# Kernel optimization log

Measured on AMD Instinct MI355X. Metric: run time of the kernel, lower is better.

The kernel has to match this reference:

```python
import jax, jax.numpy as jnp
import numpy as np

B, S, D, H, K = 64, 512, 256, 4, 1  # batch, seq, dim, heads, seeds; key_dim == D (Keras quirk)
EPS = 1e-6


def setup_inputs() -> dict:
    key = jax.random.key(0)
    ks = jax.random.split(key, 12)
    s = 1.0 / np.sqrt(D)
    return {
        "x": jax.random.normal(ks[0], (B, S, D), jnp.float32),
        "mask": jax.random.randint(ks[1], (B, S), 0, 2, jnp.int32),
        "seeds": jax.random.normal(ks[2], (K, D), jnp.float32) * s,
        "Wq": jax.random.normal(ks[3], (D, H, D), jnp.float32) * s,
        "bq": jnp.zeros((H, D), jnp.float32),
        "Wk": jax.random.normal(ks[4], (D, H, D), jnp.float32) * s,
        "bk": jnp.zeros((H, D), jnp.float32),
        "Wv": jax.random.normal(ks[5], (D, H, D), jnp.float32) * s,
        "bv": jnp.zeros((H, D), jnp.float32),
        "Wo": jax.random.normal(ks[6], (H, D, D), jnp.float32) * s,
        "bo": jnp.zeros((D,), jnp.float32),
        "gamma": jnp.ones((D,), jnp.float32),
        "beta": jnp.zeros((D,), jnp.float32),
    }


def reference(x, mask, seeds, Wq, bq, Wk, bk, Wv, bv, Wo, bo, gamma, beta):
    # Projections (Keras MHA: per-head dim = key_dim = D)
    q = jnp.einsum("kd,dhe->khe", seeds, Wq) + bq           # [K,H,D] (shared across batch)
    kp = jnp.einsum("bsd,dhe->bshe", x, Wk) + bk            # [B,S,H,D]
    vp = jnp.einsum("bsd,dhe->bshe", x, Wv) + bv            # [B,S,H,D]
    scores = jnp.einsum("khe,bshe->bhks", q, kp) / jnp.sqrt(jnp.float32(D))  # [B,H,K,S]
    adder = (1.0 - mask.astype(scores.dtype))[:, None, None, :] * -1e9
    attn = jax.nn.softmax(scores + adder, axis=-1)
    o = jnp.einsum("bhks,bshe->bkhe", attn, vp)             # [B,K,H,D]
    h = jnp.einsum("bkhe,hed->bkd", o, Wo) + bo             # attention output
    h = seeds[None] + h                                     # residual (dropout off: inference)
    mu = jnp.mean(h, axis=-1, keepdims=True)
    var = jnp.mean(jnp.square(h - mu), axis=-1, keepdims=True)
    h = (h - mu) / jnp.sqrt(var + EPS) * gamma + beta
    return h[:, 0, :]                                       # [B,D]
```

## Files before the change

### kernel.cpp

```cpp
#include <hip/hip_runtime.h>
#include <hip/hip_bf16.h>
#include <math.h>

#define BB 64
#define SS 512
#define DD 256
#define HH 4
#define SCALE 0.0625f
#define PAD 261

__device__ inline float wave_red_sum(float v) {
#pragma unroll
    for (int off = 32; off > 0; off >>= 1) v += __shfl_xor(v, off, 64);
    return v;
}
__device__ inline float wave_red_max(float v) {
#pragma unroll
    for (int off = 32; off > 0; off >>= 1) v = fmaxf(v, __shfl_xor(v, off, 64));
    return v;
}

__global__ __launch_bounds__(256) void qp_kernel(const float* __restrict__ seeds,
                                                 const float* __restrict__ Wq,
                                                 float* __restrict__ qp) {
    int c = blockIdx.x, tid = threadIdx.x;
    __shared__ float sl[16];
    if (tid < 16) sl[tid] = seeds[c * 16 + tid];
    __syncthreads();
#pragma unroll
    for (int rep = 0; rep < 4; ++rep) {
        int i = tid + rep * 256;
        float acc = 0.f;
#pragma unroll
        for (int dl = 0; dl < 16; ++dl)
            acc += sl[dl] * Wq[(size_t)(c * 16 + dl) * (HH * DD) + i];
        qp[c * (HH * DD) + i] = acc;
    }
}

__global__ __launch_bounds__(256) void kqf_kernel(const float* __restrict__ Wk,
                                                  const float* __restrict__ bk,
                                                  const float* __restrict__ bq,
                                                  const float* __restrict__ qp,
                                                  float* __restrict__ kqf,
                                                  float* __restrict__ kbg) {
    int h = blockIdx.x >> 2, ds = blockIdx.x & 3;
    int tid = threadIdx.x, w = tid >> 6, lane = tid & 63;
    __shared__ float ql[DD];
    __shared__ float red[4][64];
    __shared__ float rb[4];
    float qv = bq[h * DD + tid];
#pragma unroll
    for (int c = 0; c < 16; ++c) qv += qp[c * (HH * DD) + h * DD + tid];
    ql[tid] = qv;
    float bkv = bk[h * DD + tid] * qv;
    float t1 = wave_red_sum(bkv);
    if (lane == 0) rb[w] = t1;
    __syncthreads();
    if (tid == 0) kbg[h] = rb[0] + rb[1] + rb[2] + rb[3];
    int dl = tid & 63, ec = tid >> 6;
    int d = ds * 64 + dl;
    const float4* wrow = reinterpret_cast<const float4*>(Wk + (size_t)d * (HH * DD) + h * DD + ec * 64);
    const float4* qq4 = reinterpret_cast<const float4*>(&ql[ec * 64]);
    float acc = 0.f;
#pragma unroll
    for (int e4 = 0; e4 < 16; ++e4) {
        float4 wv = wrow[e4], qq = qq4[e4];
        acc += wv.x * qq.x + wv.y * qq.y + wv.z * qq.z + wv.w * qq.w;
    }
    red[ec][dl] = acc;
    __syncthreads();
    if (tid < 64) kqf[h * DD + ds * 64 + tid] = red[0][tid] + red[1][tid] + red[2][tid] + red[3][tid];
}

__global__ __launch_bounds__(256) void flash_kernel(const float* __restrict__ x,
                                                    const int* __restrict__ mask,
                                                    const float* __restrict__ kqg,
                                                    const float* __restrict__ kbg,
                                                    float* __restrict__ xp,
                                                    float* __restrict__ mt,
                                                    float* __restrict__ lt) {
    int b = blockIdx.x >> 3, st = blockIdx.x & 7;
    int tid = threadIdx.x, w = tid >> 6, lane = tid & 63;
    __shared__ float xt[64][PAD];
    __shared__ __align__(16) float part[4][2][64];
    float* sc = &part[0][0][0];

    const float4* xg = reinterpret_cast<const float4*>(x + ((size_t)b * SS + st * 64) * DD);
#pragma unroll
    for (int c = 0; c < 16; ++c) {
        int f = c * 256 + tid;
        float4 v = xg[f];
        int row = f >> 6, col = (f & 63) * 4;
        xt[row][col + 0] = v.x;
        xt[row][col + 1] = v.y;
        xt[row][col + 2] = v.z;
        xt[row][col + 3] = v.w;
    }
    __syncthreads();

    int s = lane;
    int hp = w >> 1, kk = w & 1;
    int off = __builtin_amdgcn_readfirstlane(hp * 2 * DD + kk * 128);
    const float* kA = kqg + off;
    const float* kB = kqg + off + DD;
    const float* xrow = &xt[s][kk * 128];
    float a0 = 0.f, a1 = 0.f;
#pragma unroll 16
    for (int k = 0; k < 128; ++k) {
        float xv = xrow[k];
        a0 = fmaf(xv, kA[k], a0);
        a1 = fmaf(xv, kB[k], a1);
    }
    part[w][0][s] = a0;
    part[w][1][s] = a1;
    __syncthreads();

    int h = w;
    float v = part[2 * (h >> 1)][h & 1][s] + part[2 * (h >> 1) + 1][h & 1][s];
    float score = (v + kbg[h]) * SCALE + (1.f - (float)mask[b * SS + st * 64 + s]) * -1e9f;
    float m = wave_red_max(score);
    float p = __expf(score - m);
    float l = wave_red_sum(p);
    __syncthreads();
    sc[h * 64 + s] = p;
    if (lane == 0) {
        mt[blockIdx.x * 4 + h] = m;
        lt[blockIdx.x * 4 + h] = l;
    }
    __syncthreads();

    float o0 = 0.f, o1 = 0.f, o2 = 0.f, o3 = 0.f;
#pragma unroll 4
    for (int sb = 0; sb < 16; ++sb) {
        float4 p0 = *reinterpret_cast<const float4*>(&sc[0 * 64 + 4 * sb]);
        float4 p1 = *reinterpret_cast<const float4*>(&sc[1 * 64 + 4 * sb]);
        float4 p2 = *reinterpret_cast<const float4*>(&sc[2 * 64 + 4 * sb]);
        float4 p3 = *reinterpret_cast<const float4*>(&sc[3 * 64 + 4 * sb]);
#pragma unroll
        for (int j = 0; j < 4; ++j) {
            float xv = xt[4 * sb + j][tid];
            float pj0 = (j == 0) ? p0.x : (j == 1) ? p0.y : (j == 2) ? p0.z : p0.w;
            float pj1 = (j == 0) ? p1.x : (j == 1) ? p1.y : (j == 2) ? p1.z : p1.w;
            float pj2 = (j == 0) ? p2.x : (j == 1) ? p2.y : (j == 2) ? p2.z : p2.w;
            float pj3 = (j == 0) ? p3.x : (j == 1) ? p3.y : (j == 2) ? p3.z : p3.w;
            o0 = fmaf(pj0, xv, o0);
            o1 = fmaf(pj1, xv, o1);
            o2 = fmaf(pj2, xv, o2);
            o3 = fmaf(pj3, xv, o3);
        }
    }
    float* xpo = xp + (size_t)blockIdx.x * 4 * DD;
    xpo[0 * DD + tid] = o0;
    xpo[1 * DD + tid] = o1;
    xpo[2 * DD + tid] = o2;
    xpo[3 * DD + tid] = o3;
}

__global__ __launch_bounds__(256) void ovwo_kernel(const float* __restrict__ xp,
                                                   const float* __restrict__ mt,
                                                   const float* __restrict__ lt,
                                                   const float* __restrict__ Wv,
                                                   const float* __restrict__ bv,
                                                   const float* __restrict__ Wo,
                                                   float* __restrict__ wop) {
    int b = blockIdx.x >> 2, h = blockIdx.x & 3;
    int tid = threadIdx.x;
    __shared__ float xl[DD];
    __shared__ float ol[DD];
    float M = -3.0e38f;
#pragma unroll
    for (int t = 0; t < 8; ++t) M = fmaxf(M, mt[(b * 8 + t) * 4 + h]);
    float L = 0.f;
    float co[8];
#pragma unroll
    for (int t = 0; t < 8; ++t) {
        co[t] = __expf(mt[(b * 8 + t) * 4 + h] - M);
        L += lt[(b * 8 + t) * 4 + h] * co[t];
    }
    float invL = 1.0f / L;
    float xb = 0.f;
#pragma unroll
    for (int t = 0; t < 8; ++t) xb += co[t] * xp[((size_t)(b * 8 + t) * 4 + h) * DD + tid];
    xl[tid] = xb * invL;
    __syncthreads();
    float acc = bv[h * DD + tid];
    const float* wv = Wv + h * DD + tid;
#pragma unroll 8
    for (int d = 0; d < DD; ++d) acc += xl[d] * wv[(size_t)d * (HH * DD)];
    ol[tid] = acc;
    __syncthreads();
    float a2 = 0.f;
    const float* wo = Wo + (size_t)(h * DD) * DD + tid;
#pragma unroll 8
    for (int e = 0; e < DD; ++e) a2 += ol[e] * wo[(size_t)e * DD];
    wop[((size_t)(b * HH + h)) * DD + tid] = a2;
}

__global__ __launch_bounds__(256) void ln_kernel(const float* __restrict__ wop,
                                                 const float* __restrict__ bo,
                                                 const float* __restrict__ seeds,
                                                 const float* __restrict__ gamma,
                                                 const float* __restrict__ beta,
                                                 float* __restrict__ out) {
    __shared__ float r1[4], r2[4];
    int b = blockIdx.x, tid = threadIdx.x;
    int w = tid >> 6, lane = tid & 63;
    float acc = bo[tid] + seeds[tid];
#pragma unroll
    for (int h = 0; h < HH; ++h) acc += wop[((size_t)(b * HH + h)) * DD + tid];

    float t = wave_red_sum(acc);
    if (lane == 0) r1[w] = t;
    __syncthreads();
    float mu = (r1[0] + r1[1] + r1[2] + r1[3]) * (1.0f / DD);
    float dv = acc - mu;
    float t2 = wave_red_sum(dv * dv);
    if (lane == 0) r2[w] = t2;
    __syncthreads();
    float var = (r2[0] + r2[1] + r2[2] + r2[3]) * (1.0f / DD);
    out[(size_t)b * DD + tid] = dv * rsqrtf(var + 1e-6f) * gamma[tid] + beta[tid];
}

extern "C" void kernel_launch(void* const* d_in, const int* in_sizes, int n_in,
                              void* d_out, int out_size, void* d_ws, size_t ws_size,
                              hipStream_t stream) {
    const float* x = (const float*)d_in[0];
    const int* mask = (const int*)d_in[1];
    const float* seeds = (const float*)d_in[2];
    const float* Wq = (const float*)d_in[3];
    const float* bq = (const float*)d_in[4];
    const float* Wk = (const float*)d_in[5];
    const float* bk = (const float*)d_in[6];
    const float* Wv = (const float*)d_in[7];
    const float* bv = (const float*)d_in[8];
    const float* Wo = (const float*)d_in[9];
    const float* bo = (const float*)d_in[10];
    const float* gamma = (const float*)d_in[11];
    const float* beta = (const float*)d_in[12];
    float* out = (float*)d_out;

    float* ws = (float*)d_ws;
    float* qp  = ws;
    float* kqf = ws + 16384;
    float* kbg = ws + 17408;
    float* mt  = ws + 17424;
    float* lt  = ws + 19472;
    float* xp  = ws + 21520;
    float* wop = ws + 545808;

    qp_kernel<<<16, 256, 0, stream>>>(seeds, Wq, qp);
    kqf_kernel<<<16, 256, 0, stream>>>(Wk, bk, bq, qp, kqf, kbg);
    flash_kernel<<<BB * 8, 256, 0, stream>>>(x, mask, kqf, kbg, xp, mt, lt);
    ovwo_kernel<<<BB * HH, 256, 0, stream>>>(xp, mt, lt, Wv, bv, Wo, wop);
    ln_kernel<<<BB, 256, 0, stream>>>(wop, bo, seeds, gamma, beta, out);
}
```

Measured before the change: 140.7 us.

## Fuse all five stages into one cooperative kernel with grid syncs

Merges the query projection, key-query fold, flash partial attention, value/output projection and layernorm into one cooperative kernel of 512 blocks, separated by grid-wide barriers. The x tile load now overlaps the query/key folding done by the first 16 blocks. The separate qp stage is merged into the kqf stage, so each of those 16 blocks computes its full query projection over all 256 seed dimensions. This is meant to remove four kernel launch gaps and the tail latency between them. In exchange it adds grid.sync costs, depends on all 512 blocks being co-resident, and leaves most blocks idle during the later stages.

```diff
diff --git a/kernel.cpp b/kernel.cpp
--- a/kernel.cpp
+++ b/kernel.cpp
@@ -1,6 +1,8 @@
 #include <hip/hip_runtime.h>
-#include <hip/hip_bf16.h>
+#include <hip/hip_cooperative_groups.h>
 #include <math.h>
+
+namespace cg = cooperative_groups;
 
 #define BB 64
 #define SS 512
@@ -20,70 +22,27 @@
     return v;
 }
 
-__global__ __launch_bounds__(256) void qp_kernel(const float* __restrict__ seeds,
-                                                 const float* __restrict__ Wq,
-                                                 float* __restrict__ qp) {
-    int c = blockIdx.x, tid = threadIdx.x;
-    __shared__ float sl[16];
-    if (tid < 16) sl[tid] = seeds[c * 16 + tid];
-    __syncthreads();
-#pragma unroll
-    for (int rep = 0; rep < 4; ++rep) {
-        int i = tid + rep * 256;
-        float acc = 0.f;
-#pragma unroll
-        for (int dl = 0; dl < 16; ++dl)
-            acc += sl[dl] * Wq[(size_t)(c * 16 + dl) * (HH * DD) + i];
-        qp[c * (HH * DD) + i] = acc;
-    }
-}
-
-__global__ __launch_bounds__(256) void kqf_kernel(const float* __restrict__ Wk,
-                                                  const float* __restrict__ bk,
-                                                  const float* __restrict__ bq,
-                                                  const float* __restrict__ qp,
-                                                  float* __restrict__ kqf,
-                                                  float* __restrict__ kbg) {
-    int h = blockIdx.x >> 2, ds = blockIdx.x & 3;
-    int tid = threadIdx.x, w = tid >> 6, lane = tid & 63;
-    __shared__ float ql[DD];
+__global__ __launch_bounds__(256) void fused_kernel(
+    const float* __restrict__ x, const int* __restrict__ mask,
+    const float* __restrict__ seeds,
+    const float* __restrict__ Wq, const float* __restrict__ bq,
+    const float* __restrict__ Wk, const float* __restrict__ bk,
+    const float* __restrict__ Wv, const float* __restrict__ bv,
+    const float* __restrict__ Wo, const float* __restrict__ bo,
+    const float* __restrict__ gamma, const float* __restrict__ beta,
+    float* __restrict__ out,
+    float* __restrict__ kqf, float* __restrict__ kbg,
+    float* __restrict__ xp, float* __restrict__ mt, float* __restrict__ lt,
+    float* __restrict__ wop) {
+    cg::grid_group grid = cg::this_grid();
+    int blk = blockIdx.x, tid = threadIdx.x, w = tid >> 6, lane = tid & 63;
+    int b = blk >> 3, st = blk & 7;
+
+    __shared__ __align__(16) float xt[64][PAD];
+    __shared__ __align__(16) float part[4][2][64];
+    __shared__ __align__(16) float ql[DD];
     __shared__ float red[4][64];
     __shared__ float rb[4];
-    float qv = bq[h * DD + tid];
-#pragma unroll
-    for (int c = 0; c < 16; ++c) qv += qp[c * (HH * DD) + h * DD + tid];
-    ql[tid] = qv;
-    float bkv = bk[h * DD + tid] * qv;
-    float t1 = wave_red_sum(bkv);
-    if (lane == 0) rb[w] = t1;
-    __syncthreads();
-    if (tid == 0) kbg[h] = rb[0] + rb[1] + rb[2] + rb[3];
-    int dl = tid & 63, ec = tid >> 6;
-    int d = ds * 64 + dl;
-    const float4* wrow = reinterpret_cast<const float4*>(Wk + (size_t)d * (HH * DD) + h * DD + ec * 64);
-    const float4* qq4 = reinterpret_cast<const float4*>(&ql[ec * 64]);
-    float acc = 0.f;
-#pragma unroll
-    for (int e4 = 0; e4 < 16; ++e4) {
-        float4 wv = wrow[e4], qq = qq4[e4];
-        acc += wv.x * qq.x + wv.y * qq.y + wv.z * qq.z + wv.w * qq.w;
-    }
-    red[ec][dl] = acc;
-    __syncthreads();
-    if (tid < 64) kqf[h * DD + ds * 64 + tid] = red[0][tid] + red[1][tid] + red[2][tid] + red[3][tid];
-}
-
-__global__ __launch_bounds__(256) void flash_kernel(const float* __restrict__ x,
-                                                    const int* __restrict__ mask,
-                                                    const float* __restrict__ kqg,
-                                                    const float* __restrict__ kbg,
-                                                    float* __restrict__ xp,
-                                                    float* __restrict__ mt,
-                                                    float* __restrict__ lt) {
-    int b = blockIdx.x >> 3, st = blockIdx.x & 7;
-    int tid = threadIdx.x, w = tid >> 6, lane = tid & 63;
-    __shared__ float xt[64][PAD];
-    __shared__ __align__(16) float part[4][2][64];
     float* sc = &part[0][0][0];
 
     const float4* xg = reinterpret_cast<const float4*>(x + ((size_t)b * SS + st * 64) * DD);
@@ -97,129 +56,147 @@
         xt[row][col + 2] = v.z;
         xt[row][col + 3] = v.w;
     }
-    __syncthreads();
-
-    int s = lane;
-    int hp = w >> 1, kk = w & 1;
-    int off = __builtin_amdgcn_readfirstlane(hp * 2 * DD + kk * 128);
-    const float* kA = kqg + off;
-    const float* kB = kqg + off + DD;
-    const float* xrow = &xt[s][kk * 128];
-    float a0 = 0.f, a1 = 0.f;
+
+    if (blk < 16) {
+        int h = blk >> 2, ds = blk & 3;
+        float qv = bq[h * DD + tid];
+#pragma unroll 8
+        for (int d = 0; d < DD; ++d)
+            qv = fmaf(seeds[d], Wq[(size_t)d * (HH * DD) + h * DD + tid], qv);
+        ql[tid] = qv;
+        float t1 = wave_red_sum(bk[h * DD + tid] * qv);
+        if (lane == 0) rb[w] = t1;
+        __syncthreads();
+        if (tid == 0) kbg[h] = rb[0] + rb[1] + rb[2] + rb[3];
+        int dl = tid & 63, ec = tid >> 6;
+        int d = ds * 64 + dl;
+        const float4* wrow = reinterpret_cast<const float4*>(Wk + (size_t)d * (HH * DD) + h * DD + ec * 64);
+        const float4* qq4 = reinterpret_cast<const float4*>(&ql[ec * 64]);
+        float acc = 0.f;
+#pragma unroll
+        for (int e4 = 0; e4 < 16; ++e4) {
+            float4 wv = wrow[e4], qq = qq4[e4];
+            acc += wv.x * qq.x + wv.y * qq.y + wv.z * qq.z + wv.w * qq.w;
+        }
+        red[ec][dl] = acc;
+        __syncthreads();
+        if (tid < 64) kqf[h * DD + ds * 64 + tid] = red[0][tid] + red[1][tid] + red[2][tid] + red[3][tid];
+    }
+    __threadfence();
+    grid.sync();
+
+    {
+        int s = lane;
+        int hp = w >> 1, kk = w & 1;
+        int off = __builtin_amdgcn_readfirstlane(hp * 2 * DD + kk * 128);
+        const float* kA = kqf + off;
+        const float* kB = kqf + off + DD;
+        const float* xrow = &xt[s][kk * 128];
+        float a0 = 0.f, a1 = 0.f;
 #pragma unroll 16
-    for (int k = 0; k < 128; ++k) {
-        float xv = xrow[k];
-        a0 = fmaf(xv, kA[k], a0);
-        a1 = fmaf(xv, kB[k], a1);
-    }
-    part[w][0][s] = a0;
-    part[w][1][s] = a1;
-    __syncthreads();
-
-    int h = w;
-    float v = part[2 * (h >> 1)][h & 1][s] + part[2 * (h >> 1) + 1][h & 1][s];
-    float score = (v + kbg[h]) * SCALE + (1.f - (float)mask[b * SS + st * 64 + s]) * -1e9f;
-    float m = wave_red_max(score);
-    float p = __expf(score - m);
-    float l = wave_red_sum(p);
-    __syncthreads();
-    sc[h * 64 + s] = p;
-    if (lane == 0) {
-        mt[blockIdx.x * 4 + h] = m;
-        lt[blockIdx.x * 4 + h] = l;
-    }
-    __syncthreads();
-
-    float o0 = 0.f, o1 = 0.f, o2 = 0.f, o3 = 0.f;
+        for (int k = 0; k < 128; ++k) {
+            float xv = xrow[k];
+            a0 = fmaf(xv, kA[k], a0);
+            a1 = fmaf(xv, kB[k], a1);
+        }
+        part[w][0][s] = a0;
+        part[w][1][s] = a1;
+        __syncthreads();
+
+        int h = w;
+        float v = part[2 * (h >> 1)][h & 1][s] + part[2 * (h >> 1) + 1][h & 1][s];
+        float score = (v + kbg[h]) * SCALE + (1.f - (float)mask[b * SS + st * 64 + s]) * -1e9f;
+        float m = wave_red_max(score);
+        float p = __expf(score - m);
+        float l = wave_red_sum(p);
+        __syncthreads();
+        sc[h * 64 + s] = p;
+        if (lane == 0) {
+            mt[blk * 4 + h] = m;
+            lt[blk * 4 + h] = l;
+        }
+        __syncthreads();
+
+        float o0 = 0.f, o1 = 0.f, o2 = 0.f, o3 = 0.f;
 #pragma unroll 4
-    for (int sb = 0; sb < 16; ++sb) {
-        float4 p0 = *reinterpret_cast<const float4*>(&sc[0 * 64 + 4 * sb]);
-        float4 p1 = *reinterpret_cast<const float4*>(&sc[1 * 64 + 4 * sb]);
-        float4 p2 = *reinterpret_cast<const float4*>(&sc[2 * 64 + 4 * sb]);
-        float4 p3 = *reinterpret_cast<const float4*>(&sc[3 * 64 + 4 * sb]);
-#pragma unroll
-        for (int j = 0; j < 4; ++j) {
-            float xv = xt[4 * sb + j][tid];
-            float pj0 = (j == 0) ? p0.x : (j == 1) ? p0.y : (j == 2) ? p0.z : p0.w;
-            float pj1 = (j == 0) ? p1.x : (j == 1) ? p1.y : (j == 2) ? p1.z : p1.w;
-            float pj2 = (j == 0) ? p2.x : (j == 1) ? p2.y : (j == 2) ? p2.z : p2.w;
-            float pj3 = (j == 0) ? p3.x : (j == 1) ? p3.y : (j == 2) ? p3.z : p3.w;
-            o0 = fmaf(pj0, xv, o0);
-            o1 = fmaf(pj1, xv, o1);
-            o2 = fmaf(pj2, xv, o2);
-            o3 = fmaf(pj3, xv, o3);
-        }
-    }
-    float* xpo = xp + (size_t)blockIdx.x * 4 * DD;
-    xpo[0 * DD + tid] = o0;
-    xpo[1 * DD + tid] = o1;
-    xpo[2 * DD + tid] = o2;
-    xpo[3 * DD + tid] = o3;
-}
-
-__global__ __launch_bounds__(256) void ovwo_kernel(const float* __restrict__ xp,
-                                                   const float* __restrict__ mt,
-                                                   const float* __restrict__ lt,
-                                                   const float* __restrict__ Wv,
-                                                   const float* __restrict__ bv,
-                                                   const float* __restrict__ Wo,
-                                                   float* __restrict__ wop) {
-    int b = blockIdx.x >> 2, h = blockIdx.x & 3;
-    int tid = threadIdx.x;
-    __shared__ float xl[DD];
-    __shared__ float ol[DD];
-    float M = -3.0e38f;
-#pragma unroll
-    for (int t = 0; t < 8; ++t) M = fmaxf(M, mt[(b * 8 + t) * 4 + h]);
-    float L = 0.f;
-    float co[8];
-#pragma unroll
-    for (int t = 0; t < 8; ++t) {
-        co[t] = __expf(mt[(b * 8 + t) * 4 + h] - M);
-        L += lt[(b * 8 + t) * 4 + h] * co[t];
-    }
-    float invL = 1.0f / L;
-    float xb = 0.f;
-#pragma unroll
-    for (int t = 0; t < 8; ++t) xb += co[t] * xp[((size_t)(b * 8 + t) * 4 + h) * DD + tid];
-    xl[tid] = xb * invL;
-    __syncthreads();
-    float acc = bv[h * DD + tid];
-    const float* wv = Wv + h * DD + tid;
+        for (int sb = 0; sb < 16; ++sb) {
+            float4 p0 = *reinterpret_cast<const float4*>(&sc[0 * 64 + 4 * sb]);
+            float4 p1 = *reinterpret_cast<const float4*>(&sc[1 * 64 + 4 * sb]);
+            float4 p2 = *reinterpret_cast<const float4*>(&sc[2 * 64 + 4 * sb]);
+            float4 p3 = *reinterpret_cast<const float4*>(&sc[3 * 64 + 4 * sb]);
+#pragma unroll
+            for (int j = 0; j < 4; ++j) {
+                float xv = xt[4 * sb + j][tid];
+                float pj0 = (j == 0) ? p0.x : (j == 1) ? p0.y : (j == 2) ? p0.z : p0.w;
+                float pj1 = (j == 0) ? p1.x : (j == 1) ? p1.y : (j == 2) ? p1.z : p1.w;
+                float pj2 = (j == 0) ? p2.x : (j == 1) ? p2.y : (j == 2) ? p2.z : p2.w;
+                float pj3 = (j == 0) ? p3.x : (j == 1) ? p3.y : (j == 2) ? p3.z : p3.w;
+                o0 = fmaf(pj0, xv, o0);
+                o1 = fmaf(pj1, xv, o1);
+                o2 = fmaf(pj2, xv, o2);
+                o3 = fmaf(pj3, xv, o3);
+            }
+        }
+        float* xpo = xp + (size_t)blk * 4 * DD;
+        xpo[0 * DD + tid] = o0;
+        xpo[1 * DD + tid] = o1;
+        xpo[2 * DD + tid] = o2;
+        xpo[3 * DD + tid] = o3;
+    }
+    __threadfence();
+    grid.sync();
+
+    if (blk < 256) {
+        int b2 = blk >> 2, h2 = blk & 3;
+        float* xl = ql;
+        float* ol = sc;
+        float M = -3.0e38f;
+#pragma unroll
+        for (int t = 0; t < 8; ++t) M = fmaxf(M, mt[(b2 * 8 + t) * 4 + h2]);
+        float L = 0.f;
+        float co[8];
+#pragma unroll
+        for (int t = 0; t < 8; ++t) {
+            co[t] = __expf(mt[(b2 * 8 + t) * 4 + h2] - M);
+            L += lt[(b2 * 8 + t) * 4 + h2] * co[t];
+        }
+        float invL = 1.0f / L;
+        float xb = 0.f;
+#pragma unroll
+        for (int t = 0; t < 8; ++t) xb += co[t] * xp[((size_t)(b2 * 8 + t) * 4 + h2) * DD + tid];
+        xl[tid] = xb * invL;
+        __syncthreads();
+        float acc = bv[h2 * DD + tid];
+        const float* wv = Wv + h2 * DD + tid;
 #pragma unroll 8
-    for (int d = 0; d < DD; ++d) acc += xl[d] * wv[(size_t)d * (HH * DD)];
-    ol[tid] = acc;
-    __syncthreads();
-    float a2 = 0.f;
-    const float* wo = Wo + (size_t)(h * DD) * DD + tid;
+        for (int d = 0; d < DD; ++d) acc = fmaf(xl[d], wv[(size_t)d * (HH * DD)], acc);
+        ol[tid] = acc;
+        __syncthreads();
+        float a2 = 0.f;
+        const float* wo = Wo + (size_t)(h2 * DD) * DD + tid;
 #pragma unroll 8
-    for (int e = 0; e < DD; ++e) a2 += ol[e] * wo[(size_t)e * DD];
-    wop[((size_t)(b * HH + h)) * DD + tid] = a2;
-}
-
-__global__ __launch_bounds__(256) void ln_kernel(const float* __restrict__ wop,
-                                                 const float* __restrict__ bo,
-                                                 const float* __restrict__ seeds,
-                                                 const float* __restrict__ gamma,
-                                                 const float* __restrict__ beta,
-                                                 float* __restrict__ out) {
-    __shared__ float r1[4], r2[4];
-    int b = blockIdx.x, tid = threadIdx.x;
-    int w = tid >> 6, lane = tid & 63;
-    float acc = bo[tid] + seeds[tid];
-#pragma unroll
-    for (int h = 0; h < HH; ++h) acc += wop[((size_t)(b * HH + h)) * DD + tid];
-
-    float t = wave_red_sum(acc);
-    if (lane == 0) r1[w] = t;
-    __syncthreads();
-    float mu = (r1[0] + r1[1] + r1[2] + r1[3]) * (1.0f / DD);
-    float dv = acc - mu;
-    float t2 = wave_red_sum(dv * dv);
-    if (lane == 0) r2[w] = t2;
-    __syncthreads();
-    float var = (r2[0] + r2[1] + r2[2] + r2[3]) * (1.0f / DD);
-    out[(size_t)b * DD + tid] = dv * rsqrtf(var + 1e-6f) * gamma[tid] + beta[tid];
+        for (int e = 0; e < DD; ++e) a2 = fmaf(ol[e], wo[(size_t)e * DD], a2);
+        wop[((size_t)(b2 * HH + h2)) * DD + tid] = a2;
+    }
+    __threadfence();
+    grid.sync();
+
+    if (blk < 64) {
+        float acc = bo[tid] + seeds[tid];
+#pragma unroll
+        for (int h = 0; h < HH; ++h) acc += wop[((size_t)(blk * HH + h)) * DD + tid];
+        float t = wave_red_sum(acc);
+        if (lane == 0) rb[w] = t;
+        __syncthreads();
+        float mu = (rb[0] + rb[1] + rb[2] + rb[3]) * (1.0f / DD);
+        float dv = acc - mu;
+        float t2 = wave_red_sum(dv * dv);
+        __syncthreads();
+        if (lane == 0) rb[w] = t2;
+        __syncthreads();
+        float var = (rb[0] + rb[1] + rb[2] + rb[3]) * (1.0f / DD);
+        out[(size_t)blk * DD + tid] = dv * rsqrtf(var + 1e-6f) * gamma[tid] + beta[tid];
+    }
 }
 
 extern "C" void kernel_launch(void* const* d_in, const int* in_sizes, int n_in,
@@ -241,17 +218,18 @@
     float* out = (float*)d_out;
 
     float* ws = (float*)d_ws;
-    float* qp  = ws;
-    float* kqf = ws + 16384;
-    float* kbg = ws + 17408;
-    float* mt  = ws + 17424;
-    float* lt  = ws + 19472;
-    float* xp  = ws + 21520;
-    float* wop = ws + 545808;
-
-    qp_kernel<<<16, 256, 0, stream>>>(seeds, Wq, qp);
-    kqf_kernel<<<16, 256, 0, stream>>>(Wk, bk, bq, qp, kqf, kbg);
-    flash_kernel<<<BB * 8, 256, 0, stream>>>(x, mask, kqf, kbg, xp, mt, lt);
-    ovwo_kernel<<<BB * HH, 256, 0, stream>>>(xp, mt, lt, Wv, bv, Wo, wop);
-    ln_kernel<<<BB, 256, 0, stream>>>(wop, bo, seeds, gamma, beta, out);
-}
+    float* kqf = ws;
+    float* kbg = ws + 1024;
+    float* mt  = ws + 1040;
+    float* lt  = ws + 3088;
+    float* xp  = ws + 5136;
+    float* wop = ws + 529424;
+
+    void* args[] = {(void*)&x, (void*)&mask, (void*)&seeds,
+                    (void*)&Wq, (void*)&bq, (void*)&Wk, (void*)&bk,
+                    (void*)&Wv, (void*)&bv, (void*)&Wo, (void*)&bo,
+                    (void*)&gamma, (void*)&beta, (void*)&out,
+                    (void*)&kqf, (void*)&kbg, (void*)&xp, (void*)&mt, (void*)&lt,
+                    (void*)&wop};
+    hipLaunchCooperativeKernel((void*)fused_kernel, dim3(BB * 8), dim3(256), args, 0, stream);
+}
```

Result: slower. 461.4 us (+228.0%).

## Fuse q-projection into setup kernel and swizzle flash LDS tile as float4

Applied to the files above, without the earlier changes.

Merges the separate q-projection kernel into the kqf kernel, so each block recomputes the full seeds·Wq for its head, which drops one launch and the workspace round trip. The flash kernel's shared x tile becomes an XOR-swizzled float4 array instead of a padded scalar array, so staging writes and score-phase reads use 128-bit LDS accesses without bank conflicts. The score dot product now reads kqf as float4. The fused setup does redundant Wq reads across the 4 ds blocks per head, and the P·X phase reads scalars out of swizzled float4 slots.

```diff
diff --git a/kernel.cpp b/kernel.cpp
--- a/kernel.cpp
+++ b/kernel.cpp
@@ -1,5 +1,4 @@
 #include <hip/hip_runtime.h>
-#include <hip/hip_bf16.h>
 #include <math.h>
 
 #define BB 64
@@ -7,7 +6,6 @@
 #define DD 256
 #define HH 4
 #define SCALE 0.0625f
-#define PAD 261
 
 __device__ inline float wave_red_sum(float v) {
 #pragma unroll
@@ -20,41 +18,24 @@
     return v;
 }
 
-__global__ __launch_bounds__(256) void qp_kernel(const float* __restrict__ seeds,
-                                                 const float* __restrict__ Wq,
-                                                 float* __restrict__ qp) {
-    int c = blockIdx.x, tid = threadIdx.x;
-    __shared__ float sl[16];
-    if (tid < 16) sl[tid] = seeds[c * 16 + tid];
-    __syncthreads();
-#pragma unroll
-    for (int rep = 0; rep < 4; ++rep) {
-        int i = tid + rep * 256;
-        float acc = 0.f;
-#pragma unroll
-        for (int dl = 0; dl < 16; ++dl)
-            acc += sl[dl] * Wq[(size_t)(c * 16 + dl) * (HH * DD) + i];
-        qp[c * (HH * DD) + i] = acc;
-    }
-}
-
-__global__ __launch_bounds__(256) void kqf_kernel(const float* __restrict__ Wk,
-                                                  const float* __restrict__ bk,
-                                                  const float* __restrict__ bq,
-                                                  const float* __restrict__ qp,
-                                                  float* __restrict__ kqf,
-                                                  float* __restrict__ kbg) {
-    int h = blockIdx.x >> 2, ds = blockIdx.x & 3;
-    int tid = threadIdx.x, w = tid >> 6, lane = tid & 63;
+__global__ __launch_bounds__(256) void setup_kernel(const float* __restrict__ seeds,
+                                                    const float* __restrict__ Wq,
+                                                    const float* __restrict__ bq,
+                                                    const float* __restrict__ Wk,
+                                                    const float* __restrict__ bk,
+                                                    float* __restrict__ kqf,
+                                                    float* __restrict__ kbg) {
+    int blk = blockIdx.x, tid = threadIdx.x, w = tid >> 6, lane = tid & 63;
+    int h = blk >> 2, ds = blk & 3;
     __shared__ float ql[DD];
     __shared__ float red[4][64];
     __shared__ float rb[4];
     float qv = bq[h * DD + tid];
-#pragma unroll
-    for (int c = 0; c < 16; ++c) qv += qp[c * (HH * DD) + h * DD + tid];
+#pragma unroll 8
+    for (int d = 0; d < DD; ++d)
+        qv = fmaf(seeds[d], Wq[(size_t)d * (HH * DD) + h * DD + tid], qv);
     ql[tid] = qv;
-    float bkv = bk[h * DD + tid] * qv;
-    float t1 = wave_red_sum(bkv);
+    float t1 = wave_red_sum(bk[h * DD + tid] * qv);
     if (lane == 0) rb[w] = t1;
     __syncthreads();
     if (tid == 0) kbg[h] = rb[0] + rb[1] + rb[2] + rb[3];
@@ -75,14 +56,14 @@
 
 __global__ __launch_bounds__(256) void flash_kernel(const float* __restrict__ x,
                                                     const int* __restrict__ mask,
-                                                    const float* __restrict__ kqg,
+                                                    const float* __restrict__ kqf,
                                                     const float* __restrict__ kbg,
                                                     float* __restrict__ xp,
                                                     float* __restrict__ mt,
                                                     float* __restrict__ lt) {
-    int b = blockIdx.x >> 3, st = blockIdx.x & 7;
-    int tid = threadIdx.x, w = tid >> 6, lane = tid & 63;
-    __shared__ float xt[64][PAD];
+    int blk = blockIdx.x, tid = threadIdx.x, w = tid >> 6, lane = tid & 63;
+    int b = blk >> 3, st = blk & 7;
+    __shared__ __align__(16) float4 xt4[64][64];
     __shared__ __align__(16) float part[4][2][64];
     float* sc = &part[0][0][0];
 
@@ -90,71 +71,76 @@
 #pragma unroll
     for (int c = 0; c < 16; ++c) {
         int f = c * 256 + tid;
-        float4 v = xg[f];
-        int row = f >> 6, col = (f & 63) * 4;
-        xt[row][col + 0] = v.x;
-        xt[row][col + 1] = v.y;
-        xt[row][col + 2] = v.z;
-        xt[row][col + 3] = v.w;
-    }
-    __syncthreads();
-
-    int s = lane;
-    int hp = w >> 1, kk = w & 1;
-    int off = __builtin_amdgcn_readfirstlane(hp * 2 * DD + kk * 128);
-    const float* kA = kqg + off;
-    const float* kB = kqg + off + DD;
-    const float* xrow = &xt[s][kk * 128];
-    float a0 = 0.f, a1 = 0.f;
-#pragma unroll 16
-    for (int k = 0; k < 128; ++k) {
-        float xv = xrow[k];
-        a0 = fmaf(xv, kA[k], a0);
-        a1 = fmaf(xv, kB[k], a1);
-    }
-    part[w][0][s] = a0;
-    part[w][1][s] = a1;
-    __syncthreads();
-
-    int h = w;
-    float v = part[2 * (h >> 1)][h & 1][s] + part[2 * (h >> 1) + 1][h & 1][s];
-    float score = (v + kbg[h]) * SCALE + (1.f - (float)mask[b * SS + st * 64 + s]) * -1e9f;
-    float m = wave_red_max(score);
-    float p = __expf(score - m);
-    float l = wave_red_sum(p);
-    __syncthreads();
-    sc[h * 64 + s] = p;
-    if (lane == 0) {
-        mt[blockIdx.x * 4 + h] = m;
-        lt[blockIdx.x * 4 + h] = l;
-    }
-    __syncthreads();
-
-    float o0 = 0.f, o1 = 0.f, o2 = 0.f, o3 = 0.f;
+        int row = f >> 6, ch = f & 63;
+        xt4[row][ch ^ (row & 7)] = xg[f];
+    }
+    __syncthreads();
+
+    {
+        int s = lane;
+        int hp = w >> 1, kk = w & 1;
+        int off = __builtin_amdgcn_readfirstlane(hp * 2 * DD + kk * 128);
+        const float4* kA4 = reinterpret_cast<const float4*>(kqf + off);
+        const float4* kB4 = reinterpret_cast<const float4*>(kqf + off + DD);
+        int sx = s & 7;
+        float a0 = 0.f, a1 = 0.f;
+#pragma unroll
+        for (int k4 = 0; k4 < 32; ++k4) {
+            float4 xv = xt4[s][(kk * 32 + k4) ^ sx];
+            float4 av = kA4[k4], bv = kB4[k4];
+            a0 += xv.x * av.x + xv.y * av.y + xv.z * av.z + xv.w * av.w;
+            a1 += xv.x * bv.x + xv.y * bv.y + xv.z * bv.z + xv.w * bv.w;
+        }
+        part[w][0][s] = a0;
+        part[w][1][s] = a1;
+    }
+    __syncthreads();
+
+    {
+        int s = lane, h = w;
+        float v = part[2 * (h >> 1)][h & 1][s] + part[2 * (h >> 1) + 1][h & 1][s];
+        float score = (v + kbg[h]) * SCALE + (1.f - (float)mask[b * SS + st * 64 + s]) * -1e9f;
+        float m = wave_red_max(score);
+        float p = __expf(score - m);
+        float l = wave_red_sum(p);
+        __syncthreads();
+        sc[h * 64 + s] = p;
+        if (lane == 0) {
+            mt[blk * 4 + h] = m;
+            lt[blk * 4 + h] = l;
+        }
+    }
+    __syncthreads();
+
+    {
+        float o0 = 0.f, o1 = 0.f, o2 = 0.f, o3 = 0.f;
+        int ch = tid >> 2, sub = tid & 3;
 #pragma unroll 4
-    for (int sb = 0; sb < 16; ++sb) {
-        float4 p0 = *reinterpret_cast<const float4*>(&sc[0 * 64 + 4 * sb]);
-        float4 p1 = *reinterpret_cast<const float4*>(&sc[1 * 64 + 4 * sb]);
-        float4 p2 = *reinterpret_cast<const float4*>(&sc[2 * 64 + 4 * sb]);
-        float4 p3 = *reinterpret_cast<const float4*>(&sc[3 * 64 + 4 * sb]);
-#pragma unroll
-        for (int j = 0; j < 4; ++j) {
-            float xv = xt[4 * sb + j][tid];
-            float pj0 = (j == 0) ? p0.x : (j == 1) ? p0.y : (j == 2) ? p0.z : p0.w;
-            float pj1 = (j == 0) ? p1.x : (j == 1) ? p1.y : (j == 2) ? p1.z : p1.w;
-            float pj2 = (j == 0) ? p2.x : (j == 1) ? p2.y : (j == 2) ? p2.z : p2.w;
-            float pj3 = (j == 0) ? p3.x : (j == 1) ? p3.y : (j == 2) ? p3.z : p3.w;
-            o0 = fmaf(pj0, xv, o0);
-            o1 = fmaf(pj1, xv, o1);
-            o2 = fmaf(pj2, xv, o2);
-            o3 = fmaf(pj3, xv, o3);
+        for (int sb = 0; sb < 16; ++sb) {
+            float4 p0 = *reinterpret_cast<const float4*>(&sc[0 * 64 + 4 * sb]);
+            float4 p1 = *reinterpret_cast<const float4*>(&sc[1 * 64 + 4 * sb]);
+            float4 p2 = *reinterpret_cast<const float4*>(&sc[2 * 64 + 4 * sb]);
+            float4 p3 = *reinterpret_cast<const float4*>(&sc[3 * 64 + 4 * sb]);
+#pragma unroll
+            for (int j = 0; j < 4; ++j) {
+                int row = 4 * sb + j;
+                float xv = reinterpret_cast<const float*>(&xt4[row][ch ^ (row & 7)])[sub];
+                float pj0 = (j == 0) ? p0.x : (j == 1) ? p0.y : (j == 2) ? p0.z : p0.w;
+                float pj1 = (j == 0) ? p1.x : (j == 1) ? p1.y : (j == 2) ? p1.z : p1.w;
+                float pj2 = (j == 0) ? p2.x : (j == 1) ? p2.y : (j == 2) ? p2.z : p2.w;
+                float pj3 = (j == 0) ? p3.x : (j == 1) ? p3.y : (j == 2) ? p3.z : p3.w;
+                o0 = fmaf(pj0, xv, o0);
+                o1 = fmaf(pj1, xv, o1);
+                o2 = fmaf(pj2, xv, o2);
+                o3 = fmaf(pj3, xv, o3);
+            }
         }
-    }
-    float* xpo = xp + (size_t)blockIdx.x * 4 * DD;
-    xpo[0 * DD + tid] = o0;
-    xpo[1 * DD + tid] = o1;
-    xpo[2 * DD + tid] = o2;
-    xpo[3 * DD + tid] = o3;
+        float* xpo = xp + (size_t)blk * 4 * DD;
+        xpo[0 * DD + tid] = o0;
+        xpo[1 * DD + tid] = o1;
+        xpo[2 * DD + tid] = o2;
+        xpo[3 * DD + tid] = o3;
+    }
 }
 
 __global__ __launch_bounds__(256) void ovwo_kernel(const float* __restrict__ xp,
@@ -187,13 +173,13 @@
     float acc = bv[h * DD + tid];
     const float* wv = Wv + h * DD + tid;
 #pragma unroll 8
-    for (int d = 0; d < DD; ++d) acc += xl[d] * wv[(size_t)d * (HH * DD)];
+    for (int d = 0; d < DD; ++d) acc = fmaf(xl[d], wv[(size_t)d * (HH * DD)], acc);
     ol[tid] = acc;
     __syncthreads();
     float a2 = 0.f;
     const float* wo = Wo + (size_t)(h * DD) * DD + tid;
 #pragma unroll 8
-    for (int e = 0; e < DD; ++e) a2 += ol[e] * wo[(size_t)e * DD];
+    for (int e = 0; e < DD; ++e) a2 = fmaf(ol[e], wo[(size_t)e * DD], a2);
     wop[((size_t)(b * HH + h)) * DD + tid] = a2;
 }
 
@@ -209,7 +195,6 @@
     float acc = bo[tid] + seeds[tid];
 #pragma unroll
     for (int h = 0; h < HH; ++h) acc += wop[((size_t)(b * HH + h)) * DD + tid];
-
     float t = wave_red_sum(acc);
     if (lane == 0) r1[w] = t;
     __syncthreads();
@@ -241,16 +226,14 @@
     float* out = (float*)d_out;
 
     float* ws = (float*)d_ws;
-    float* qp  = ws;
-    float* kqf = ws + 16384;
-    float* kbg = ws + 17408;
-    float* mt  = ws + 17424;
-    float* lt  = ws + 19472;
-    float* xp  = ws + 21520;
-    float* wop = ws + 545808;
-
-    qp_kernel<<<16, 256, 0, stream>>>(seeds, Wq, qp);
-    kqf_kernel<<<16, 256, 0, stream>>>(Wk, bk, bq, qp, kqf, kbg);
+    float* kqf = ws;
+    float* kbg = ws + 1024;
+    float* mt  = ws + 1040;
+    float* lt  = ws + 3088;
+    float* xp  = ws + 5136;
+    float* wop = ws + 529424;
+
+    setup_kernel<<<16, 256, 0, stream>>>(seeds, Wq, bq, Wk, bk, kqf, kbg);
     flash_kernel<<<BB * 8, 256, 0, stream>>>(x, mask, kqf, kbg, xp, mt, lt);
     ovwo_kernel<<<BB * HH, 256, 0, stream>>>(xp, mt, lt, Wv, bv, Wo, wop);
     ln_kernel<<<BB, 256, 0, stream>>>(wop, bo, seeds, gamma, beta, out);
```

Result: no change. 141.5 us (+0.6%).
